# Performance work log

Measured on AMD Instinct MI355X. Metric: run time of the kernel, lower is better.

Reference implementation:

```python
import jax, jax.numpy as jnp
import numpy as np
import math

EMBED_DIM = 2048
NUM_HEADS = 16
VID_DIM = 2048
NUM_VID = 10
HEAD_DIM = EMBED_DIM // NUM_HEADS
EPS = 1e-5


def _layernorm(x, g, b):
    mu = jnp.mean(x, axis=-1, keepdims=True)
    var = jnp.mean((x - mu) ** 2, axis=-1, keepdims=True)
    return (x - mu) * jax.lax.rsqrt(var + EPS) * g + b


def setup_inputs() -> dict:
    key = jax.random.key(0)
    ks = jax.random.split(key, 12)
    B = 8192
    inp = {
        "speech_token": jax.random.normal(ks[0], (B, 1, EMBED_DIM), jnp.float32),
        "video_tokens": jax.random.normal(ks[1], (B, NUM_VID, VID_DIM), jnp.float32),
        # LayerNorm params
        "ln_s_g": jnp.ones((EMBED_DIM,), jnp.float32),
        "ln_s_b": jnp.zeros((EMBED_DIM,), jnp.float32),
        "ln_v_g": jnp.ones((VID_DIM,), jnp.float32),
        "ln_v_b": jnp.zeros((VID_DIM,), jnp.float32),
        # projections, stored as [in, out]
        "Wq": jax.random.normal(ks[2], (EMBED_DIM, EMBED_DIM), jnp.float32) * 0.02,
        "bq": jnp.zeros((EMBED_DIM,), jnp.float32),
        "Wk": jax.random.normal(ks[3], (VID_DIM, EMBED_DIM), jnp.float32) * 0.02,
        "bk": jnp.zeros((EMBED_DIM,), jnp.float32),
        "Wv": jax.random.normal(ks[4], (VID_DIM, EMBED_DIM), jnp.float32) * 0.02,
        "bv": jnp.zeros((EMBED_DIM,), jnp.float32),
        "Wo": jax.random.normal(ks[5], (EMBED_DIM, EMBED_DIM), jnp.float32) * 0.02,
        "bo": jnp.zeros((EMBED_DIM,), jnp.float32),
        "alpha": jnp.float32(0.005),
    }
    return inp


def reference(speech_token, video_tokens, ln_s_g, ln_s_b, ln_v_g, ln_v_b,
              Wq, bq, Wk, bk, Wv, bv, Wo, bo, alpha):
    B = speech_token.shape[0]
    sp = _layernorm(speech_token, ln_s_g, ln_s_b)          # [B,1,E]
    vt = _layernorm(video_tokens, ln_v_g, ln_v_b)          # [B,K,E]

    positions = jnp.arange(NUM_VID, dtype=jnp.float32)
    pos_bias = jnp.clip(-alpha * positions ** 2, -10.0, 0.0)  # [K]
    pos_bias = pos_bias.reshape(1, 1, 1, NUM_VID)

    Q = (sp @ Wq + bq).reshape(B, 1, NUM_HEADS, HEAD_DIM).transpose(0, 2, 1, 3)
    K = (vt @ Wk + bk).reshape(B, NUM_VID, NUM_HEADS, HEAD_DIM).transpose(0, 2, 1, 3)
    V = (vt @ Wv + bv).reshape(B, NUM_VID, NUM_HEADS, HEAD_DIM).transpose(0, 2, 1, 3)

    scores = jnp.einsum("bhqd,bhkd->bhqk", Q, K) / math.sqrt(HEAD_DIM)
    scores = jnp.clip(scores, -1000.0, 1000.0) + pos_bias
    attn_probs = jax.nn.softmax(scores, axis=-1)           # [B,H,1,K]
    context = jnp.einsum("bhqk,bhkd->bhqd", attn_probs, V)  # [B,H,1,hd]
    context = context.transpose(0, 2, 1, 3).reshape(B, 1, EMBED_DIM)
    output = context @ Wo + bo                             # [B,1,E]
    return (output, attn_probs)
```

## Files before the change

### kernel.cpp

```cpp
#include <hip/hip_runtime.h>


#define B_TOT 8192
#define E     2048
#define NH    16
#define HD    128
#define KV    10

typedef short bf16x8 __attribute__((ext_vector_type(8)));
typedef float f32x4  __attribute__((ext_vector_type(4)));

__device__ __forceinline__ unsigned short f2bf(float f) {
  unsigned int u = __float_as_uint(f);
  u = (u + 0x7fffu + ((u >> 16) & 1u)) >> 16;
  return (unsigned short)u;
}
__device__ __forceinline__ float bf2f(unsigned short h) {
  return __uint_as_float(((unsigned int)h) << 16);
}
__device__ __forceinline__ void unpack8(int4 v, float* f) {
  unsigned int x = (unsigned int)v.x, y = (unsigned int)v.y;
  unsigned int z = (unsigned int)v.z, w = (unsigned int)v.w;
  f[0] = __uint_as_float(x << 16); f[1] = __uint_as_float(x & 0xffff0000u);
  f[2] = __uint_as_float(y << 16); f[3] = __uint_as_float(y & 0xffff0000u);
  f[4] = __uint_as_float(z << 16); f[5] = __uint_as_float(z & 0xffff0000u);
  f[6] = __uint_as_float(w << 16); f[7] = __uint_as_float(w & 0xffff0000u);
}
__device__ __forceinline__ void async16(const void* g, void* l) {
  __builtin_amdgcn_global_load_lds(
      (const __attribute__((address_space(1))) unsigned int*)g,
      (__attribute__((address_space(3))) unsigned int*)l, 16, 0, 0);
}

__global__ __launch_bounds__(256) void ln_speech_kernel(
    const float* __restrict__ x, const float* __restrict__ g,
    const float* __restrict__ bb, unsigned short* __restrict__ out)
{
  __shared__ float red[8];
  const int tid = threadIdx.x, wave = tid >> 6, lane = tid & 63;
  const long b = blockIdx.x;
  const float4* row = (const float4*)(x + b * E);
  float4 a0 = row[tid], a1 = row[tid + 256];
  float s  = a0.x + a0.y + a0.z + a0.w + a1.x + a1.y + a1.z + a1.w;
  float s2 = a0.x*a0.x + a0.y*a0.y + a0.z*a0.z + a0.w*a0.w
           + a1.x*a1.x + a1.y*a1.y + a1.z*a1.z + a1.w*a1.w;
  #pragma unroll
  for (int off = 32; off; off >>= 1) { s += __shfl_xor(s, off); s2 += __shfl_xor(s2, off); }
  if (lane == 0) { red[wave] = s; red[wave + 4] = s2; }
  __syncthreads();
  s  = red[0] + red[1] + red[2] + red[3];
  s2 = red[4] + red[5] + red[6] + red[7];
  const float mu = s * (1.0f / E);
  const float rs = rsqrtf(s2 * (1.0f / E) - mu * mu + 1e-5f);
  const float4* g4 = (const float4*)g;
  const float4* b4 = (const float4*)bb;
  ushort4* o = (ushort4*)(out + b * E);
  {
    float4 gg = g4[tid], bv = b4[tid];
    ushort4 r;
    r.x = f2bf((a0.x - mu) * rs * gg.x + bv.x);
    r.y = f2bf((a0.y - mu) * rs * gg.y + bv.y);
    r.z = f2bf((a0.z - mu) * rs * gg.z + bv.z);
    r.w = f2bf((a0.w - mu) * rs * gg.w + bv.w);
    o[tid] = r;
  }
  {
    float4 gg = g4[tid + 256], bv = b4[tid + 256];
    ushort4 r;
    r.x = f2bf((a1.x - mu) * rs * gg.x + bv.x);
    r.y = f2bf((a1.y - mu) * rs * gg.y + bv.y);
    r.z = f2bf((a1.z - mu) * rs * gg.z + bv.z);
    r.w = f2bf((a1.w - mu) * rs * gg.w + bv.w);
    o[tid + 256] = r;
  }
}

__global__ __launch_bounds__(256) void wtrans_kernel(
    const float* __restrict__ Wq, const float* __restrict__ Wv, const float* __restrict__ Wo,
    unsigned short* __restrict__ WqT, unsigned short* __restrict__ WvT, unsigned short* __restrict__ WoT)
{
  __shared__ float t[32][33];
  const float* W; unsigned short* WT;
  if (blockIdx.z == 0)      { W = Wq; WT = WqT; }
  else if (blockIdx.z == 1) { W = Wv; WT = WvT; }
  else                      { W = Wo; WT = WoT; }
  const int tx = threadIdx.x, ty = threadIdx.y;
  const int n0 = blockIdx.x * 32, k0 = blockIdx.y * 32;
  #pragma unroll
  for (int j = 0; j < 4; j++)
    t[ty + 8*j][tx] = W[(long)(k0 + ty + 8*j) * E + n0 + tx];
  __syncthreads();
  #pragma unroll
  for (int j = 0; j < 4; j++)
    WT[(long)(n0 + ty + 8*j) * E + k0 + tx] = f2bf(t[tx][ty + 8*j]);
}

__global__ __launch_bounds__(256) void wcast_kernel(
    const float* __restrict__ W, unsigned short* __restrict__ Wb)
{
  const long i = ((long)blockIdx.x * 256 + threadIdx.x) * 4;
  float4 v = *(const float4*)(W + i);
  ushort4 o;
  o.x = f2bf(v.x); o.y = f2bf(v.y); o.z = f2bf(v.z); o.w = f2bf(v.w);
  *(ushort4*)(Wb + i) = o;
}

template<bool OUT_BF16, bool HAS_BIAS>
__global__ __launch_bounds__(256) void gemm_bt_kernel(
    const unsigned short* __restrict__ A, int lda, long sAz,
    const unsigned short* __restrict__ BT, int ldb, long sBz,
    void* __restrict__ Cv, int ldc, long sCz,
    const float* __restrict__ bias, int sBiasz, int Ksize)
{
  __shared__ unsigned short As[128 * 32];
  __shared__ unsigned short Bs[128 * 32];
  const int tid = threadIdx.x, wave = tid >> 6, lane = tid & 63;
  A  += (long)blockIdx.z * sAz;
  BT += (long)blockIdx.z * sBz;
  const int tileM = blockIdx.x * 128, tileN = blockIdx.y * 128;
  const int r0 = wave * 16 + (lane >> 2);
  const int cb = (lane & 3) * 8;
  const unsigned short* Ag0 = A  + (long)(tileM + r0) * lda + cb;
  const unsigned short* Ag1 = A  + (long)(tileM + r0 + 64) * lda + cb;
  const unsigned short* Bg0 = BT + (long)(tileN + r0) * ldb + cb;
  const unsigned short* Bg1 = BT + (long)(tileN + r0 + 64) * ldb + cb;
  unsigned short* As0 = As + wave * 512;
  unsigned short* As1 = As + (wave + 4) * 512;
  unsigned short* Bs0 = Bs + wave * 512;
  unsigned short* Bs1 = Bs + (wave + 4) * 512;
  const int wm = wave & 1, wn = wave >> 1;
  const int quad = lane >> 4, l15 = lane & 15;
  const unsigned short* Ard = As + (wm * 64 + l15) * 32 + quad * 8;
  const unsigned short* Brd = Bs + (wn * 64 + l15) * 32 + quad * 8;

  f32x4 acc[4][4] = {};

  for (int k0 = 0; k0 < Ksize; k0 += 32) {
    __syncthreads();
    async16(Ag0 + k0, As0);
    async16(Ag1 + k0, As1);
    async16(Bg0 + k0, Bs0);
    async16(Bg1 + k0, Bs1);
    __syncthreads();
    bf16x8 af[4], bfv[4];
    #pragma unroll
    for (int im = 0; im < 4; im++) af[im]  = *(const bf16x8*)(Ard + im * 512);
    #pragma unroll
    for (int in = 0; in < 4; in++) bfv[in] = *(const bf16x8*)(Brd + in * 512);
    #pragma unroll
    for (int im = 0; im < 4; im++)
      #pragma unroll
      for (int in = 0; in < 4; in++)
        acc[im][in] = __builtin_amdgcn_mfma_f32_16x16x32_bf16(af[im], bfv[in], acc[im][in], 0, 0, 0);
  }

  const long czoff = (long)blockIdx.z * sCz;
  #pragma unroll
  for (int in = 0; in < 4; in++) {
    const int gn = tileN + wn * 64 + in * 16 + l15;
    const float badd = HAS_BIAS ? bias[(long)blockIdx.z * sBiasz + gn] : 0.0f;
    #pragma unroll
    for (int im = 0; im < 4; im++) {
      const int gm = tileM + wm * 64 + im * 16 + quad * 4;
      #pragma unroll
      for (int r = 0; r < 4; r++) {
        const float v = acc[im][in][r] + badd;
        const long off = czoff + (long)(gm + r) * ldc + gn;
        if (OUT_BF16) ((unsigned short*)Cv)[off] = f2bf(v);
        else          ((float*)Cv)[off] = v;
      }
    }
  }
}

__global__ __launch_bounds__(256) void attn_kernel(
    const float* __restrict__ video, const float* __restrict__ lvg,
    const float* __restrict__ lvb,
    const unsigned short* __restrict__ Qb, const float* __restrict__ bk,
    unsigned short* __restrict__ U, float* __restrict__ probs,
    const float* __restrict__ alphap, int b_base)
{
  __shared__ unsigned short vs[KV][E];
  const int tid = threadIdx.x, wave = tid >> 6, lane = tid & 63;
  const int bl = blockIdx.x;
  const long b = (long)b_base + bl;
  const float alpha = alphap[0];

  for (int k = wave; k < KV; k += 4) {
    const float4* row = (const float4*)(video + (b * KV + k) * E);
    float4 xv[8];
    float s = 0.f, s2 = 0.f;
    #pragma unroll
    for (int it = 0; it < 8; it++) {
      xv[it] = row[lane + it * 64];
      s  += xv[it].x + xv[it].y + xv[it].z + xv[it].w;
      s2 += xv[it].x*xv[it].x + xv[it].y*xv[it].y + xv[it].z*xv[it].z + xv[it].w*xv[it].w;
    }
    #pragma unroll
    for (int off = 32; off; off >>= 1) { s += __shfl_xor(s, off); s2 += __shfl_xor(s2, off); }
    const float mu = s * (1.0f / E);
    const float rs = rsqrtf(s2 * (1.0f / E) - mu * mu + 1e-5f);
    #pragma unroll
    for (int it = 0; it < 8; it++) {
      const int i4 = lane + it * 64;
      float4 gg = ((const float4*)lvg)[i4];
      float4 bb = ((const float4*)lvb)[i4];
      ushort4 o;
      o.x = f2bf((xv[it].x - mu) * rs * gg.x + bb.x);
      o.y = f2bf((xv[it].y - mu) * rs * gg.y + bb.y);
      o.z = f2bf((xv[it].z - mu) * rs * gg.z + bb.z);
      o.w = f2bf((xv[it].w - mu) * rs * gg.w + bb.w);
      ((ushort4*)&vs[k][0])[i4] = o;
    }
  }
  __syncthreads();

  float acc[4][KV];
  #pragma unroll
  for (int hh = 0; hh < 4; hh++)
    #pragma unroll
    for (int k = 0; k < KV; k++) acc[hh][k] = 0.f;
  float qdb[4];
  #pragma unroll
  for (int hh = 0; hh < 4; hh++) {
    const int h = wave + hh * 4;
    const float q0 = bf2f(Qb[b * E + h * HD + lane]);
    const float q1 = bf2f(Qb[b * E + h * HD + 64 + lane]);
    qdb[hh] = q0 * bk[h * HD + lane] + q1 * bk[h * HD + 64 + lane];
  }
  for (int it = 0; it < 4; it++) {
    const int i0 = lane * 8 + it * 512;
    float uf[4][8];
    #pragma unroll
    for (int hh = 0; hh < 4; hh++) {
      const int h = wave + hh * 4;
      int4 uv = *(const int4*)(U + ((long)bl * NH + h) * E + i0);
      unpack8(uv, uf[hh]);
    }
    #pragma unroll
    for (int k = 0; k < KV; k++) {
      int4 vv = *(const int4*)&vs[k][i0];
      float vf[8]; unpack8(vv, vf);
      #pragma unroll
      for (int hh = 0; hh < 4; hh++)
        #pragma unroll
        for (int j = 0; j < 8; j++)
          acc[hh][k] += uf[hh][j] * vf[j];
    }
  }
  #pragma unroll
  for (int off = 32; off; off >>= 1) {
    #pragma unroll
    for (int hh = 0; hh < 4; hh++) {
      #pragma unroll
      for (int k = 0; k < KV; k++) acc[hh][k] += __shfl_xor(acc[hh][k], off);
      qdb[hh] += __shfl_xor(qdb[hh], off);
    }
  }

  const float rsd = 0.088388347648318447f;
  float p[4][KV];
  #pragma unroll
  for (int hh = 0; hh < 4; hh++) {
    float mx = -1e30f;
    #pragma unroll
    for (int k = 0; k < KV; k++) {
      float sc = (acc[hh][k] + qdb[hh]) * rsd;
      sc = fminf(fmaxf(sc, -1000.f), 1000.f);
      sc += fmaxf(-alpha * (float)(k * k), -10.f);
      p[hh][k] = sc;
      mx = fmaxf(mx, sc);
    }
    float sum = 0.f;
    #pragma unroll
    for (int k = 0; k < KV; k++) { p[hh][k] = __expf(p[hh][k] - mx); sum += p[hh][k]; }
    const float inv = 1.0f / sum;
    #pragma unroll
    for (int k = 0; k < KV; k++) p[hh][k] *= inv;
  }
  if (lane < KV) {
    #pragma unroll
    for (int hh = 0; hh < 4; hh++) {
      const int h = wave + hh * 4;
      float pv = 0.f;
      #pragma unroll
      for (int k = 0; k < KV; k++) if (k == lane) pv = p[hh][k];
      probs[(b * NH + h) * KV + lane] = pv;
    }
  }

  for (int it = 0; it < 4; it++) {
    const int i0 = lane * 8 + it * 512;
    float pv[4][8];
    #pragma unroll
    for (int hh = 0; hh < 4; hh++)
      #pragma unroll
      for (int j = 0; j < 8; j++) pv[hh][j] = 0.f;
    #pragma unroll
    for (int k = 0; k < KV; k++) {
      int4 vv = *(const int4*)&vs[k][i0];
      float vf[8]; unpack8(vv, vf);
      #pragma unroll
      for (int hh = 0; hh < 4; hh++)
        #pragma unroll
        for (int j = 0; j < 8; j++)
          pv[hh][j] += p[hh][k] * vf[j];
    }
    #pragma unroll
    for (int hh = 0; hh < 4; hh++) {
      const int h = wave + hh * 4;
      unsigned int w0 = (unsigned int)f2bf(pv[hh][0]) | ((unsigned int)f2bf(pv[hh][1]) << 16);
      unsigned int w1 = (unsigned int)f2bf(pv[hh][2]) | ((unsigned int)f2bf(pv[hh][3]) << 16);
      unsigned int w2 = (unsigned int)f2bf(pv[hh][4]) | ((unsigned int)f2bf(pv[hh][5]) << 16);
      unsigned int w3 = (unsigned int)f2bf(pv[hh][6]) | ((unsigned int)f2bf(pv[hh][7]) << 16);
      int4 st; st.x = (int)w0; st.y = (int)w1; st.z = (int)w2; st.w = (int)w3;
      *(int4*)(U + ((long)bl * NH + h) * E + i0) = st;
    }
  }
}

extern "C" void kernel_launch(void* const* d_in, const int* in_sizes, int n_in,
                              void* d_out, int out_size, void* d_ws, size_t ws_size,
                              hipStream_t stream) {
  const float* speech = (const float*)d_in[0];
  const float* video  = (const float*)d_in[1];
  const float* ln_s_g = (const float*)d_in[2];
  const float* ln_s_b = (const float*)d_in[3];
  const float* ln_v_g = (const float*)d_in[4];
  const float* ln_v_b = (const float*)d_in[5];
  const float* Wq = (const float*)d_in[6];
  const float* bq = (const float*)d_in[7];
  const float* Wk = (const float*)d_in[8];
  const float* bk = (const float*)d_in[9];
  const float* Wv = (const float*)d_in[10];
  const float* bv = (const float*)d_in[11];
  const float* Wo = (const float*)d_in[12];
  const float* bo = (const float*)d_in[13];
  const float* alphap = (const float*)d_in[14];

  char* ws = (char*)d_ws;
  unsigned short* sN  = (unsigned short*)(ws);
  unsigned short* Qb  = (unsigned short*)(ws + 33554432);
  unsigned short* ctx = (unsigned short*)(ws + 67108864);
  unsigned short* WqT = (unsigned short*)(ws + 100663296);
  unsigned short* WvT = (unsigned short*)(ws + 109051904);
  unsigned short* WoT = (unsigned short*)(ws + 117440512);
  unsigned short* Wkb = (unsigned short*)(ws + 125829120);
  unsigned short* U   = (unsigned short*)(ws + 134217728);

  float* out0  = (float*)d_out;
  float* probs = out0 + (long)B_TOT * E;

  const size_t fixed = 134217728;
  long rows_cap = 0;
  if (ws_size > fixed) rows_cap = (long)((ws_size - fixed) / ((size_t)NH * E * 2));
  int chunk = (int)((rows_cap / 128) * 128);
  if (chunk > B_TOT) chunk = B_TOT;
  if (chunk < 128)   chunk = 128;

  ln_speech_kernel<<<B_TOT, 256, 0, stream>>>(speech, ln_s_g, ln_s_b, sN);
  wtrans_kernel<<<dim3(64, 64, 3), dim3(32, 8), 0, stream>>>(Wq, Wv, Wo, WqT, WvT, WoT);
  wcast_kernel<<<4096, 256, 0, stream>>>(Wk, Wkb);

  gemm_bt_kernel<true, true><<<dim3(64, 16, 1), 256, 0, stream>>>(
      sN, E, 0, WqT, E, 0, Qb, E, 0, bq, 0, E);

  for (int b0 = 0; b0 < B_TOT; b0 += chunk) {
    const int rows = (B_TOT - b0 < chunk) ? (B_TOT - b0) : chunk;
    gemm_bt_kernel<true, false><<<dim3(rows / 128, 16, NH), 256, 0, stream>>>(
        Qb + (long)b0 * E, E, HD, Wkb, E, HD, U, NH * E, E, nullptr, 0, HD);
    attn_kernel<<<rows, 256, 0, stream>>>(video, ln_v_g, ln_v_b, Qb, bk, U, probs, alphap, b0);
    gemm_bt_kernel<true, true><<<dim3(rows / 128, 1, NH), 256, 0, stream>>>(
        U, NH * E, E, WvT, E, (long)HD * E, ctx + (long)b0 * E, E, HD, bv, HD, E);
  }

  gemm_bt_kernel<false, true><<<dim3(64, 16, 1), 256, 0, stream>>>(
      ctx, E, 0, WoT, E, 0, out0, E, 0, bo, 0, E);
}
```

Measured before the change: 1.928 ms.

## Compute attention scores with MFMA and loop heads inside U GEMM blocks

The score dot products (U · normalized video) move from scalar FMAs with shuffle reductions to bf16 MFMA instructions. Video rows are padded to 16 in LDS, and partial scores are reduced across waves through shared memory. Softmax now runs on 16 threads, and video row loads are double-buffered. The U GEMM becomes a dedicated kernel that loops over all heads within each block instead of launching a head grid dimension, which adds serial work per block but reuses the tile addressing.

```diff
diff --git a/kernel.cpp b/kernel.cpp
--- a/kernel.cpp
+++ b/kernel.cpp
@@ -6,6 +6,7 @@
 #define NH    16
 #define HD    128
 #define KV    10
+#define VSP   2056
 
 typedef short bf16x8 __attribute__((ext_vector_type(8)));
 typedef float f32x4  __attribute__((ext_vector_type(4)));
@@ -173,28 +174,114 @@
   }
 }
 
-__global__ __launch_bounds__(256) void attn_kernel(
+__global__ __launch_bounds__(256) void u_gemm_kernel(
+    const unsigned short* __restrict__ Qb,
+    const unsigned short* __restrict__ Wkb,
+    unsigned short* __restrict__ U)
+{
+  __shared__ unsigned short As[128 * 32];
+  __shared__ unsigned short Bs[128 * 32];
+  const int tid = threadIdx.x, wave = tid >> 6, lane = tid & 63;
+  const int tileM = blockIdx.x * 128, tileN = blockIdx.y * 128;
+  const int r0 = wave * 16 + (lane >> 2);
+  const int cb = (lane & 3) * 8;
+  const unsigned short* Ag0 = Qb  + (long)(tileM + r0) * E + cb;
+  const unsigned short* Ag1 = Qb  + (long)(tileM + r0 + 64) * E + cb;
+  const unsigned short* Bg0 = Wkb + (long)(tileN + r0) * E + cb;
+  const unsigned short* Bg1 = Wkb + (long)(tileN + r0 + 64) * E + cb;
+  unsigned short* As0 = As + wave * 512;
+  unsigned short* As1 = As + (wave + 4) * 512;
+  unsigned short* Bs0 = Bs + wave * 512;
+  unsigned short* Bs1 = Bs + (wave + 4) * 512;
+  const int wm = wave & 1, wn = wave >> 1;
+  const int quad = lane >> 4, l15 = lane & 15;
+  const unsigned short* Ard = As + (wm * 64 + l15) * 32 + quad * 8;
+  const unsigned short* Brd = Bs + (wn * 64 + l15) * 32 + quad * 8;
+
+  for (int h = 0; h < NH; h++) {
+    f32x4 acc[4][4] = {};
+    const int hoff = h * HD;
+    #pragma unroll
+    for (int k0 = 0; k0 < HD; k0 += 32) {
+      __syncthreads();
+      async16(Ag0 + hoff + k0, As0);
+      async16(Ag1 + hoff + k0, As1);
+      async16(Bg0 + hoff + k0, Bs0);
+      async16(Bg1 + hoff + k0, Bs1);
+      __syncthreads();
+      bf16x8 af[4], bfv[4];
+      #pragma unroll
+      for (int im = 0; im < 4; im++) af[im]  = *(const bf16x8*)(Ard + im * 512);
+      #pragma unroll
+      for (int in = 0; in < 4; in++) bfv[in] = *(const bf16x8*)(Brd + in * 512);
+      #pragma unroll
+      for (int im = 0; im < 4; im++)
+        #pragma unroll
+        for (int in = 0; in < 4; in++)
+          acc[im][in] = __builtin_amdgcn_mfma_f32_16x16x32_bf16(af[im], bfv[in], acc[im][in], 0, 0, 0);
+    }
+    #pragma unroll
+    for (int in = 0; in < 4; in++) {
+      const int gn = tileN + wn * 64 + in * 16 + l15;
+      #pragma unroll
+      for (int im = 0; im < 4; im++) {
+        const int gm = tileM + wm * 64 + im * 16 + quad * 4;
+        #pragma unroll
+        for (int r = 0; r < 4; r++)
+          U[((long)(gm + r) * NH + h) * E + gn] = f2bf(acc[im][in][r]);
+      }
+    }
+  }
+}
+
+__global__ __launch_bounds__(256) void attn2_kernel(
     const float* __restrict__ video, const float* __restrict__ lvg,
     const float* __restrict__ lvb,
     const unsigned short* __restrict__ Qb, const float* __restrict__ bk,
-    unsigned short* __restrict__ U, float* __restrict__ probs,
+    unsigned short* U, float* __restrict__ probs,
     const float* __restrict__ alphap, int b_base)
 {
-  __shared__ unsigned short vs[KV][E];
+  __shared__ unsigned short vs[16 * VSP];
+  __shared__ float sred[4 * 256];
+  __shared__ float p_lds[16 * 16];
+  __shared__ float qdb_lds[16];
   const int tid = threadIdx.x, wave = tid >> 6, lane = tid & 63;
+  const int quad = lane >> 4, l15 = lane & 15;
   const int bl = blockIdx.x;
   const long b = (long)b_base + bl;
-  const float alpha = alphap[0];
-
-  for (int k = wave; k < KV; k += 4) {
-    const float4* row = (const float4*)(video + (b * KV + k) * E);
-    float4 xv[8];
+  const unsigned short* Ub = U + (long)bl * NH * E;
+
+  const int kcount = (wave < 2) ? 3 : 2;
+  float4 xv[2][8];
+  {
+    const float4* row = (const float4*)(video + (b * KV + wave) * E);
+    #pragma unroll
+    for (int it = 0; it < 8; it++) xv[0][it] = row[lane + it * 64];
+  }
+  const unsigned short* Uw = Ub + (long)l15 * E + wave * 512 + quad * 8;
+  int4 bfrag[4];
+  #pragma unroll
+  for (int c = 0; c < 4; c++) bfrag[c] = *(const int4*)(Uw + c * 32);
+
+  {
+    int4 z; z.x = 0; z.y = 0; z.z = 0; z.w = 0;
+    int4* dst = (int4*)(vs + 10 * VSP);
+    for (int i = tid; i < 6 * VSP / 8; i += 256) dst[i] = z;
+  }
+
+  for (int r = 0; r < kcount; r++) {
+    const int k = wave + r * 4;
+    if (r + 1 < kcount) {
+      const float4* nrow = (const float4*)(video + (b * KV + wave + (r + 1) * 4) * E);
+      #pragma unroll
+      for (int it = 0; it < 8; it++) xv[(r + 1) & 1][it] = nrow[lane + it * 64];
+    }
+    float4* xr = xv[r & 1];
     float s = 0.f, s2 = 0.f;
     #pragma unroll
     for (int it = 0; it < 8; it++) {
-      xv[it] = row[lane + it * 64];
-      s  += xv[it].x + xv[it].y + xv[it].z + xv[it].w;
-      s2 += xv[it].x*xv[it].x + xv[it].y*xv[it].y + xv[it].z*xv[it].z + xv[it].w*xv[it].w;
+      s  += xr[it].x + xr[it].y + xr[it].z + xr[it].w;
+      s2 += xr[it].x*xr[it].x + xr[it].y*xr[it].y + xr[it].z*xr[it].z + xr[it].w*xr[it].w;
     }
     #pragma unroll
     for (int off = 32; off; off >>= 1) { s += __shfl_xor(s, off); s2 += __shfl_xor(s2, off); }
@@ -206,105 +293,97 @@
       float4 gg = ((const float4*)lvg)[i4];
       float4 bb = ((const float4*)lvb)[i4];
       ushort4 o;
-      o.x = f2bf((xv[it].x - mu) * rs * gg.x + bb.x);
-      o.y = f2bf((xv[it].y - mu) * rs * gg.y + bb.y);
-      o.z = f2bf((xv[it].z - mu) * rs * gg.z + bb.z);
-      o.w = f2bf((xv[it].w - mu) * rs * gg.w + bb.w);
-      ((ushort4*)&vs[k][0])[i4] = o;
-    }
-  }
-  __syncthreads();
-
-  float acc[4][KV];
-  #pragma unroll
-  for (int hh = 0; hh < 4; hh++)
-    #pragma unroll
-    for (int k = 0; k < KV; k++) acc[hh][k] = 0.f;
-  float qdb[4];
+      o.x = f2bf((xr[it].x - mu) * rs * gg.x + bb.x);
+      o.y = f2bf((xr[it].y - mu) * rs * gg.y + bb.y);
+      o.z = f2bf((xr[it].z - mu) * rs * gg.z + bb.z);
+      o.w = f2bf((xr[it].w - mu) * rs * gg.w + bb.w);
+      ((ushort4*)&vs[k * VSP])[i4] = o;
+    }
+  }
   #pragma unroll
   for (int hh = 0; hh < 4; hh++) {
     const int h = wave + hh * 4;
     const float q0 = bf2f(Qb[b * E + h * HD + lane]);
     const float q1 = bf2f(Qb[b * E + h * HD + 64 + lane]);
-    qdb[hh] = q0 * bk[h * HD + lane] + q1 * bk[h * HD + 64 + lane];
+    float qd = q0 * bk[h * HD + lane] + q1 * bk[h * HD + 64 + lane];
+    #pragma unroll
+    for (int off = 32; off; off >>= 1) qd += __shfl_xor(qd, off);
+    if (lane == 0) qdb_lds[h] = qd;
+  }
+  __syncthreads();
+
+  const unsigned short* vsrd = vs + l15 * VSP + wave * 512 + quad * 8;
+  f32x4 sacc = {};
+  #pragma unroll
+  for (int j = 0; j < 16; j++) {
+    bf16x8 af = *(const bf16x8*)(vsrd + j * 32);
+    bf16x8 bf = *(const bf16x8*)&bfrag[j & 3];
+    sacc = __builtin_amdgcn_mfma_f32_16x16x32_bf16(af, bf, sacc, 0, 0, 0);
+    if (j + 4 < 16) bfrag[j & 3] = *(const int4*)(Uw + (j + 4) * 32);
+  }
+  #pragma unroll
+  for (int r = 0; r < 4; r++)
+    sred[wave * 256 + (quad * 4 + r) * 16 + l15] = sacc[r];
+  __syncthreads();
+
+  {
+    const float sc = sred[tid] + sred[256 + tid] + sred[512 + tid] + sred[768 + tid];
+    __syncthreads();
+    sred[tid] = sc;
+  }
+  __syncthreads();
+
+  if (tid < NH) {
+    const int h = tid;
+    const float alpha = alphap[0];
+    const float rsd = 0.088388347648318447f;
+    const float qd = qdb_lds[h];
+    float sv[KV];
+    float mx = -1e30f;
+    #pragma unroll
+    for (int k = 0; k < KV; k++) {
+      float s = (sred[k * 16 + h] + qd) * rsd;
+      s = fminf(fmaxf(s, -1000.f), 1000.f);
+      s += fmaxf(-alpha * (float)(k * k), -10.f);
+      sv[k] = s;
+      mx = fmaxf(mx, s);
+    }
+    float sum = 0.f;
+    #pragma unroll
+    for (int k = 0; k < KV; k++) { sv[k] = __expf(sv[k] - mx); sum += sv[k]; }
+    const float inv = 1.0f / sum;
+    #pragma unroll
+    for (int k = 0; k < KV; k++) {
+      const float pv = sv[k] * inv;
+      p_lds[h * 16 + k] = pv;
+      probs[(b * NH + h) * KV + k] = pv;
+    }
+  }
+  __syncthreads();
+
+  float pk[4][KV];
+  #pragma unroll
+  for (int hh = 0; hh < 4; hh++) {
+    const int h = wave + hh * 4;
+    #pragma unroll
+    for (int k = 0; k < KV; k++) pk[hh][k] = p_lds[h * 16 + k];
   }
   for (int it = 0; it < 4; it++) {
     const int i0 = lane * 8 + it * 512;
-    float uf[4][8];
-    #pragma unroll
-    for (int hh = 0; hh < 4; hh++) {
-      const int h = wave + hh * 4;
-      int4 uv = *(const int4*)(U + ((long)bl * NH + h) * E + i0);
-      unpack8(uv, uf[hh]);
-    }
+    float pv[4][8];
+    #pragma unroll
+    for (int hh = 0; hh < 4; hh++)
+      #pragma unroll
+      for (int j = 0; j < 8; j++) pv[hh][j] = 0.f;
     #pragma unroll
     for (int k = 0; k < KV; k++) {
-      int4 vv = *(const int4*)&vs[k][i0];
-      float vf[8]; unpack8(vv, vf);
+      int4 vvp = *(const int4*)&vs[k * VSP + i0];
+      float vf[8]; unpack8(vvp, vf);
       #pragma unroll
       for (int hh = 0; hh < 4; hh++)
         #pragma unroll
         for (int j = 0; j < 8; j++)
-          acc[hh][k] += uf[hh][j] * vf[j];
-    }
-  }
-  #pragma unroll
-  for (int off = 32; off; off >>= 1) {
-    #pragma unroll
-    for (int hh = 0; hh < 4; hh++) {
-      #pragma unroll
-      for (int k = 0; k < KV; k++) acc[hh][k] += __shfl_xor(acc[hh][k], off);
-      qdb[hh] += __shfl_xor(qdb[hh], off);
-    }
-  }
-
-  const float rsd = 0.088388347648318447f;
-  float p[4][KV];
-  #pragma unroll
-  for (int hh = 0; hh < 4; hh++) {
-    float mx = -1e30f;
-    #pragma unroll
-    for (int k = 0; k < KV; k++) {
-      float sc = (acc[hh][k] + qdb[hh]) * rsd;
-      sc = fminf(fmaxf(sc, -1000.f), 1000.f);
-      sc += fmaxf(-alpha * (float)(k * k), -10.f);
-      p[hh][k] = sc;
-      mx = fmaxf(mx, sc);
-    }
-    float sum = 0.f;
-    #pragma unroll
-    for (int k = 0; k < KV; k++) { p[hh][k] = __expf(p[hh][k] - mx); sum += p[hh][k]; }
-    const float inv = 1.0f / sum;
-    #pragma unroll
-    for (int k = 0; k < KV; k++) p[hh][k] *= inv;
-  }
-  if (lane < KV) {
-    #pragma unroll
-    for (int hh = 0; hh < 4; hh++) {
-      const int h = wave + hh * 4;
-      float pv = 0.f;
-      #pragma unroll
-      for (int k = 0; k < KV; k++) if (k == lane) pv = p[hh][k];
-      probs[(b * NH + h) * KV + lane] = pv;
-    }
-  }
-
-  for (int it = 0; it < 4; it++) {
-    const int i0 = lane * 8 + it * 512;
-    float pv[4][8];
-    #pragma unroll
-    for (int hh = 0; hh < 4; hh++)
-      #pragma unroll
-      for (int j = 0; j < 8; j++) pv[hh][j] = 0.f;
-    #pragma unroll
-    for (int k = 0; k < KV; k++) {
-      int4 vv = *(const int4*)&vs[k][i0];
-      float vf[8]; unpack8(vv, vf);
-      #pragma unroll
-      for (int hh = 0; hh < 4; hh++)
-        #pragma unroll
-        for (int j = 0; j < 8; j++)
-          pv[hh][j] += p[hh][k] * vf[j];
+          pv[hh][j] += pk[hh][k] * vf[j];
     }
     #pragma unroll
     for (int hh = 0; hh < 4; hh++) {
@@ -367,9 +446,9 @@
 
   for (int b0 = 0; b0 < B_TOT; b0 += chunk) {
     const int rows = (B_TOT - b0 < chunk) ? (B_TOT - b0) : chunk;
-    gemm_bt_kernel<true, false><<<dim3(rows / 128, 16, NH), 256, 0, stream>>>(
-        Qb + (long)b0 * E, E, HD, Wkb, E, HD, U, NH * E, E, nullptr, 0, HD);
-    attn_kernel<<<rows, 256, 0, stream>>>(video, ln_v_g, ln_v_b, Qb, bk, U, probs, alphap, b0);
+    u_gemm_kernel<<<dim3(rows / 128, 16), 256, 0, stream>>>(
+        Qb + (long)b0 * E, Wkb, U);
+    attn2_kernel<<<rows, 256, 0, stream>>>(video, ln_v_g, ln_v_b, Qb, bk, U, probs, alphap, b0);
     gemm_bt_kernel<true, true><<<dim3(rows / 128, 1, NH), 256, 0, stream>>>(
         U, NH * E, E, WvT, E, (long)HD * E, ctx + (long)b0 * E, E, HD, bv, HD, E);
   }
```

Result: slower. 2.091 ms (+8.5%).
